# Kernel tuning notes

Measured on AMD Instinct MI355X. Metric: run time of the kernel, lower is better.

The kernel has to match this reference:

```python
import jax, jax.numpy as jnp
import numpy as np

DIM = 512
NUM_HEADS = 4
SCALE = 1.0 / np.sqrt(DIM)  # note: module scales by 1/sqrt(dim), not 1/sqrt(head_dim)


def setup_inputs() -> dict:
    key = jax.random.key(0)
    k1, k2, k3, k4, k5, k6 = jax.random.split(key, 6)
    B, N, M, C = 8, 2048, 2048, DIM
    bound = 1.0 / np.sqrt(C)
    return {
        "F1": jax.random.normal(k1, (B, N, C), dtype=jnp.float32),
        "F2": jax.random.normal(k2, (B, M, C), dtype=jnp.float32),
        "W_qkv": jax.random.uniform(k3, (C, C), jnp.float32, -bound, bound),
        "b_qkv": jax.random.uniform(k4, (C,), jnp.float32, -bound, bound),
        "W_proj": jax.random.uniform(k5, (C, C), jnp.float32, -bound, bound),
        "b_proj": jax.random.uniform(k6, (C,), jnp.float32, -bound, bound),
    }


def reference(F1, F2, W_qkv, b_qkv, W_proj, b_proj):
    B, N, C = F1.shape
    M = F2.shape[1]
    H, D = NUM_HEADS, C // NUM_HEADS
    # shared qkv projection (same weights for q, k and v in the original module)
    q = (F1 @ W_qkv + b_qkv).reshape(B, N, H, D)  # queries from F1
    kv = (F2 @ W_qkv + b_qkv).reshape(B, M, H, D)  # keys == values from F2
    attn = jnp.einsum("bnhd,bmhd->bhnm", q * SCALE, kv)
    attn = jax.nn.softmax(attn, axis=-1)
    x = jnp.einsum("bhnm,bmhd->bnhd", attn, kv).reshape(B, N, C)
    return x @ W_proj + b_proj
```

## Files before the change

kernel.cpp:

```cpp
#include <hip/hip_runtime.h>
#include <math.h>


typedef __attribute__((ext_vector_type(8))) short s16x8;
typedef __attribute__((ext_vector_type(4))) float f32x4;

#define C_DIM 512
#define HDIM  128
#define NROWS 16384
#define SCALE_Q 0.04419417382415922f
#define LOG2E   1.4426950408889634f

__device__ __forceinline__ unsigned short f2bf(float f) {
    union { float f; unsigned u; } v; v.f = f;
    unsigned r = v.u + 0x7fffu + ((v.u >> 16) & 1u);
    return (unsigned short)(r >> 16);
}

__device__ __forceinline__ void async16(const void* g, void* l) {
    __builtin_amdgcn_global_load_lds(
        (const __attribute__((address_space(1))) void*)g,
        (__attribute__((address_space(3))) void*)l, 16, 0, 0);
}

__global__ __launch_bounds__(256)
void conv_bf16_2(const float* __restrict__ s0, const float* __restrict__ s1,
                 unsigned short* __restrict__ d0, unsigned short* __restrict__ d1,
                 int n8) {
    const float* src = blockIdx.y ? s1 : s0;
    unsigned short* dst = blockIdx.y ? d1 : d0;
    int i = blockIdx.x * 256 + threadIdx.x;
    if (i >= n8) return;
    float4 a = ((const float4*)src)[2 * i];
    float4 b = ((const float4*)src)[2 * i + 1];
    union { unsigned short us[8]; uint4 v; } o;
    o.us[0] = f2bf(a.x); o.us[1] = f2bf(a.y); o.us[2] = f2bf(a.z); o.us[3] = f2bf(a.w);
    o.us[4] = f2bf(b.x); o.us[5] = f2bf(b.y); o.us[6] = f2bf(b.z); o.us[7] = f2bf(b.w);
    ((uint4*)dst)[i] = o.v;
}

__global__ __launch_bounds__(256)
void wconv_t2(const float* __restrict__ W0, const float* __restrict__ W1,
              unsigned short* __restrict__ T0, unsigned short* __restrict__ T1) {
    const float* W = blockIdx.z ? W1 : W0;
    unsigned short* Wt = blockIdx.z ? T1 : T0;
    __shared__ float t[64][65];
    const int k0 = blockIdx.y * 64, n0 = blockIdx.x * 64;
    const int c = threadIdx.x & 63, r0 = threadIdx.x >> 6;
#pragma unroll
    for (int r = r0; r < 64; r += 4)
        t[r][c] = W[(size_t)(k0 + r) * C_DIM + n0 + c];
    __syncthreads();
#pragma unroll
    for (int r = r0; r < 64; r += 4)
        Wt[(size_t)(n0 + r) * C_DIM + k0 + c] = f2bf(t[c][r]);
}

__global__ __launch_bounds__(256)
void kv_transpose(const unsigned short* __restrict__ KV,
                  unsigned short* __restrict__ KVT) {
    __shared__ unsigned short t[64][66];
    const int key0 = blockIdx.x * 64;
    const int d0   = blockIdx.y * 64;
    const int bh   = blockIdx.z;
    const int b    = bh >> 2, h = bh & 3;
    const int c = threadIdx.x & 63, r0 = threadIdx.x >> 6;
    const unsigned short* src = KV + ((size_t)(b * 2048 + key0)) * C_DIM + h * HDIM + d0;
#pragma unroll
    for (int r = r0; r < 64; r += 4)
        t[r][c] = src[(size_t)r * C_DIM + c];
    __syncthreads();
    unsigned short* dst = KVT + ((size_t)(bh * HDIM + d0)) * 2048 + key0;
#pragma unroll
    for (int r = r0; r < 64; r += 4)
        dst[(size_t)r * 2048 + c] = t[c][r];
}

template <int OUT_BF16>
__global__ __launch_bounds__(256, 3)
void gemm_bt(const unsigned short* __restrict__ A,
             const unsigned short* __restrict__ Bt,
             const float* __restrict__ bias,
             void* __restrict__ Cv, float oscTop, int topRows) {
    __shared__ __align__(16) unsigned short As[128][64];
    __shared__ __align__(16) unsigned short Bs[128][64];

    const int tid  = threadIdx.x;
    const int wid  = tid >> 6;
    const int lane = tid & 63;
    const int lr   = lane & 15;
    const int quad = lane >> 4;
    const int wm   = wid >> 1;
    const int wn   = wid & 1;
    const int rowBase = blockIdx.y * 128;
    const int colBase = blockIdx.x * 128;
    const int srow = lane >> 3;
    const int soff = srow * C_DIM + (((lane & 7) ^ (srow & 7)) * 8);
    const float osc = (rowBase < topRows) ? oscTop : 1.0f;

    f32x4 acc[4][4];
#pragma unroll
    for (int i = 0; i < 4; i++)
#pragma unroll
        for (int j = 0; j < 4; j++) acc[i][j] = (f32x4)0.0f;

    for (int kt = 0; kt < 8; kt++) {
        const int k0 = kt * 64;
        __syncthreads();
#pragma unroll
        for (int i = 0; i < 4; i++) {
            const int R = wid * 32 + i * 8;
            async16(A  + (size_t)(rowBase + R) * C_DIM + k0 + soff, &As[R][0]);
            async16(Bt + (size_t)(colBase + R) * C_DIM + k0 + soff, &Bs[R][0]);
        }
        __syncthreads();

#pragma unroll
        for (int s = 0; s < 2; s++) {
            s16x8 af[4], bf[4];
#pragma unroll
            for (int i = 0; i < 4; i++)
                af[i] = *(const s16x8*)&As[wm * 64 + i * 16 + lr][((s * 4 + quad) ^ (lr & 7)) * 8];
#pragma unroll
            for (int j = 0; j < 4; j++)
                bf[j] = *(const s16x8*)&Bs[wn * 64 + j * 16 + lr][((s * 4 + quad) ^ (lr & 7)) * 8];
#pragma unroll
            for (int i = 0; i < 4; i++)
#pragma unroll
                for (int j = 0; j < 4; j++)
                    acc[i][j] = __builtin_amdgcn_mfma_f32_16x16x32_bf16(af[i], bf[j], acc[i][j], 0, 0, 0);
        }
    }

    float bcol[4];
#pragma unroll
    for (int j = 0; j < 4; j++)
        bcol[j] = bias[colBase + wn * 64 + j * 16 + lr];
#pragma unroll
    for (int i = 0; i < 4; i++) {
#pragma unroll
        for (int j = 0; j < 4; j++) {
            const int col = colBase + wn * 64 + j * 16 + lr;
#pragma unroll
            for (int r = 0; r < 4; r++) {
                const int row = rowBase + wm * 64 + i * 16 + quad * 4 + r;
                float v = (acc[i][j][r] + bcol[j]) * osc;
                if (OUT_BF16)
                    ((unsigned short*)Cv)[(size_t)row * C_DIM + col] = f2bf(v);
                else
                    ((float*)Cv)[(size_t)row * C_DIM + col] = v;
            }
        }
    }
}

__global__ __launch_bounds__(512, 2)
void cross_attn(const unsigned short* __restrict__ Q,
                const unsigned short* __restrict__ KV,
                const unsigned short* __restrict__ KVT,
                unsigned short* __restrict__ X) {
    __shared__ __align__(16) unsigned short Kt[4][64][128];
    __shared__ __align__(16) unsigned short Vt[4][128][64];

    const int tid  = threadIdx.x;
    const int wid  = tid >> 6;
    const int lane = tid & 63;
    const int lr   = lane & 15;
    const int quad = lane >> 4;

    const int wg   = blockIdx.x;
    const int xcd  = wg & 7;
    const int slot = wg >> 3;
    const int p    = xcd + 8 * (slot & 3);
    const int xblk = slot >> 2;
    const int b    = p >> 2;
    const int h    = p & 3;
    const int hoff = h * HDIM;
    const size_t qrow0  = (size_t)b * 2048 + xblk * 256 + wid * 32;
    const size_t kvrow0 = (size_t)b * 2048;

    s16x8 qf[2][4];
#pragma unroll
    for (int i = 0; i < 2; i++)
#pragma unroll
        for (int kk = 0; kk < 4; kk++)
            qf[i][kk] = *(const s16x8*)(Q + (qrow0 + i * 16 + lr) * C_DIM + hoff + kk * 32 + quad * 8);

    const unsigned short* pK[2];
    const unsigned short* pV[2];
#pragma unroll
    for (int a = 0; a < 2; a++) {
        const int R   = wid * 8 + a * 4 + (lane >> 4);
        const int key = 32 * (R >> 5) + 8 * ((R >> 2) & 3) + 4 * ((R >> 4) & 1) + (R & 3);
        const int pp  = lane & 15;
        const int ck  = (pp & 8) | ((pp ^ (R & 7)) & 7);
        pK[a] = KV + (kvrow0 + key) * C_DIM + hoff + ck * 8;
        const int d  = wid * 16 + a * 8 + (lane >> 3);
        const int cv = (lane & 7) ^ (lane >> 3);
        pV[a] = KVT + ((size_t)((b * 4 + h) * HDIM + d)) * 2048 + cv * 8;
    }

    f32x4 O[2][8];
#pragma unroll
    for (int i = 0; i < 2; i++)
#pragma unroll
        for (int dt = 0; dt < 8; dt++) O[i][dt] = (f32x4)0.0f;
    float lacc[2];
    lacc[0] = 0.0f; lacc[1] = 0.0f;

    auto STAGE = [&](int t, int buf) {
        const size_t key0 = (size_t)t * 64;
#pragma unroll
        for (int a = 0; a < 2; a++) {
            async16(pK[a] + key0 * C_DIM, &Kt[buf][wid * 8 + a * 4][0]);
            async16(pV[a] + key0,         &Vt[buf][wid * 16 + a * 8][0]);
        }
    };

    auto COMPUTE = [&](int cur) {
        f32x4 s[2][4];
#pragma unroll
        for (int i = 0; i < 2; i++)
#pragma unroll
            for (int j = 0; j < 4; j++) s[i][j] = (f32x4)0.0f;
        __builtin_amdgcn_s_setprio(1);
#pragma unroll
        for (int kk = 0; kk < 4; kk++) {
#pragma unroll
            for (int j = 0; j < 4; j++) {
                s16x8 kf = *(const s16x8*)&Kt[cur][j * 16 + lr][((kk * 4 + quad) ^ (lr & 7)) * 8];
                s[0][j] = __builtin_amdgcn_mfma_f32_16x16x32_bf16(kf, qf[0][kk], s[0][j], 0, 0, 0);
                s[1][j] = __builtin_amdgcn_mfma_f32_16x16x32_bf16(kf, qf[1][kk], s[1][j], 0, 0, 0);
            }
        }
        __builtin_amdgcn_s_setprio(0);

        s16x8 pa[2][2];
#pragma unroll
        for (int i = 0; i < 2; i++) {
#pragma unroll
            for (int kk = 0; kk < 2; kk++) {
                float p0 = __builtin_amdgcn_exp2f(s[i][2 * kk][0]);
                float p1 = __builtin_amdgcn_exp2f(s[i][2 * kk][1]);
                float p2 = __builtin_amdgcn_exp2f(s[i][2 * kk][2]);
                float p3 = __builtin_amdgcn_exp2f(s[i][2 * kk][3]);
                float p4 = __builtin_amdgcn_exp2f(s[i][2 * kk + 1][0]);
                float p5 = __builtin_amdgcn_exp2f(s[i][2 * kk + 1][1]);
                float p6 = __builtin_amdgcn_exp2f(s[i][2 * kk + 1][2]);
                float p7 = __builtin_amdgcn_exp2f(s[i][2 * kk + 1][3]);
                lacc[i] += ((p0 + p1) + (p2 + p3)) + ((p4 + p5) + (p6 + p7));
                union { unsigned short us[8]; s16x8 v; } pu;
                pu.us[0] = f2bf(p0); pu.us[1] = f2bf(p1);
                pu.us[2] = f2bf(p2); pu.us[3] = f2bf(p3);
                pu.us[4] = f2bf(p4); pu.us[5] = f2bf(p5);
                pu.us[6] = f2bf(p6); pu.us[7] = f2bf(p7);
                pa[i][kk] = pu.v;
            }
        }

        __builtin_amdgcn_s_setprio(1);
#pragma unroll
        for (int kk = 0; kk < 2; kk++) {
#pragma unroll
            for (int dt = 0; dt < 8; dt++) {
                s16x8 vf = *(const s16x8*)&Vt[cur][dt * 16 + lr][((kk * 4 + quad) ^ (lr & 7)) * 8];
                O[0][dt] = __builtin_amdgcn_mfma_f32_16x16x32_bf16(pa[0][kk], vf, O[0][dt], 0, 0, 0);
                O[1][dt] = __builtin_amdgcn_mfma_f32_16x16x32_bf16(pa[1][kk], vf, O[1][dt], 0, 0, 0);
            }
        }
        __builtin_amdgcn_s_setprio(0);
    };

    STAGE(0, 0);
    STAGE(1, 1);

#pragma unroll 4
    for (int kt = 0; kt < 28; kt++) {
        STAGE(kt + 2, (kt + 2) & 3);
        asm volatile("s_waitcnt vmcnt(8)" ::: "memory");
        __builtin_amdgcn_sched_barrier(0);
        __builtin_amdgcn_s_barrier();
        __builtin_amdgcn_sched_barrier(0);
        COMPUTE(kt & 3);
    }
    STAGE(30, 2);
    asm volatile("s_waitcnt vmcnt(8)" ::: "memory");
    __builtin_amdgcn_sched_barrier(0);
    __builtin_amdgcn_s_barrier();
    __builtin_amdgcn_sched_barrier(0);
    COMPUTE(0);

    STAGE(31, 3);
    asm volatile("s_waitcnt vmcnt(8)" ::: "memory");
    __builtin_amdgcn_sched_barrier(0);
    __builtin_amdgcn_s_barrier();
    __builtin_amdgcn_sched_barrier(0);
    COMPUTE(1);

    asm volatile("s_waitcnt vmcnt(4)" ::: "memory");
    __builtin_amdgcn_sched_barrier(0);
    __builtin_amdgcn_s_barrier();
    __builtin_amdgcn_sched_barrier(0);
    COMPUTE(2);

    asm volatile("s_waitcnt vmcnt(0)" ::: "memory");
    __builtin_amdgcn_sched_barrier(0);
    __builtin_amdgcn_s_barrier();
    __builtin_amdgcn_sched_barrier(0);
    COMPUTE(3);

#pragma unroll
    for (int i = 0; i < 2; i++) {
        float l = lacc[i];
        l += __shfl_xor(l, 16);
        l += __shfl_xor(l, 32);
#pragma unroll
        for (int r = 0; r < 4; r++) {
            const float inv = 1.0f / __shfl(l, quad * 4 + r);
            const size_t row = (qrow0 + i * 16 + quad * 4 + r) * C_DIM + hoff;
#pragma unroll
            for (int dt = 0; dt < 8; dt++)
                X[row + dt * 16 + lr] = f2bf(O[i][dt][r] * inv);
        }
    }
}

extern "C" void kernel_launch(void* const* d_in, const int* in_sizes, int n_in,
                              void* d_out, int out_size, void* d_ws, size_t ws_size,
                              hipStream_t stream) {
    const float* F1     = (const float*)d_in[0];
    const float* F2     = (const float*)d_in[1];
    const float* W_qkv  = (const float*)d_in[2];
    const float* b_qkv  = (const float*)d_in[3];
    const float* W_proj = (const float*)d_in[4];
    const float* b_proj = (const float*)d_in[5];
    float* out = (float*)d_out;

    const size_t NC = (size_t)NROWS * C_DIM;
    unsigned short* F1b = (unsigned short*)d_ws;
    unsigned short* F2b = F1b + NC;
    unsigned short* Qw  = F2b + NC;
    unsigned short* KVw = Qw  + NC;
    unsigned short* Wqt = KVw + NC;
    unsigned short* Wpt = Wqt + C_DIM * C_DIM;
    unsigned short* Xw  = F1b;
    unsigned short* KVT = F2b;

    dim3 blk(256);

    conv_bf16_2<<<dim3(NC / 8 / 256, 2), blk, 0, stream>>>(F1, F2, F1b, F2b, (int)(NC / 8));
    wconv_t2<<<dim3(8, 8, 2), blk, 0, stream>>>(W_qkv, W_proj, Wqt, Wpt);

    gemm_bt<1><<<dim3(4, 256), blk, 0, stream>>>(F1b, Wqt, b_qkv, Qw, SCALE_Q * LOG2E, NROWS);
    kv_transpose<<<dim3(32, 2, 32), blk, 0, stream>>>(KVw, KVT);
    cross_attn<<<dim3(256), dim3(512), 0, stream>>>(Qw, KVw, KVT, Xw);
    gemm_bt<0><<<dim3(4, 128), blk, 0, stream>>>(Xw, Wpt, b_proj, out, 1.0f, 0);
}
```

Baseline: 239.3 us.

## Double-buffer GEMM LDS tiles and remap workgroups across XCDs

The projection GEMM now keeps two LDS buffers for A and B tiles. It prefetches the next k-slice with async global-to-LDS loads while computing the current one, using a partial vmcnt wait and split barriers, and raises wave priority around the MFMA section. Grids are flattened to 1D with an XCD-aware mapping so that neighbouring row tiles sharing weight columns land on the same XCD. LDS use doubles and launch bounds drop from 3 to 2 blocks per CU, which trades occupancy for overlap.

```diff
diff --git a/kernel.cpp b/kernel.cpp
--- a/kernel.cpp
+++ b/kernel.cpp
@@ -77,13 +77,13 @@
 }
 
 template <int OUT_BF16>
-__global__ __launch_bounds__(256, 3)
+__global__ __launch_bounds__(256, 2)
 void gemm_bt(const unsigned short* __restrict__ A,
              const unsigned short* __restrict__ Bt,
              const float* __restrict__ bias,
              void* __restrict__ Cv, float oscTop, int topRows) {
-    __shared__ __align__(16) unsigned short As[128][64];
-    __shared__ __align__(16) unsigned short Bs[128][64];
+    __shared__ __align__(16) unsigned short As[2][128][64];
+    __shared__ __align__(16) unsigned short Bs[2][128][64];
 
     const int tid  = threadIdx.x;
     const int wid  = tid >> 6;
@@ -92,8 +92,15 @@
     const int quad = lane >> 4;
     const int wm   = wid >> 1;
     const int wn   = wid & 1;
-    const int rowBase = blockIdx.y * 128;
-    const int colBase = blockIdx.x * 128;
+
+    const int wg   = blockIdx.x;
+    const int xcd  = wg & 7;
+    const int s_   = wg >> 3;
+    const int xblk = s_ & 3;
+    const int y    = xcd + 8 * (s_ >> 2);
+    const int rowBase = y * 128;
+    const int colBase = xblk * 128;
+
     const int srow = lane >> 3;
     const int soff = srow * C_DIM + (((lane & 7) ^ (srow & 7)) * 8);
     const float osc = (rowBase < topRows) ? oscTop : 1.0f;
@@ -104,32 +111,52 @@
 #pragma unroll
         for (int j = 0; j < 4; j++) acc[i][j] = (f32x4)0.0f;
 
-    for (int kt = 0; kt < 8; kt++) {
+    auto STAGE = [&](int kt, int buf) {
         const int k0 = kt * 64;
-        __syncthreads();
 #pragma unroll
         for (int i = 0; i < 4; i++) {
             const int R = wid * 32 + i * 8;
-            async16(A  + (size_t)(rowBase + R) * C_DIM + k0 + soff, &As[R][0]);
-            async16(Bt + (size_t)(colBase + R) * C_DIM + k0 + soff, &Bs[R][0]);
-        }
-        __syncthreads();
-
+            async16(A  + (size_t)(rowBase + R) * C_DIM + k0 + soff, &As[buf][R][0]);
+            async16(Bt + (size_t)(colBase + R) * C_DIM + k0 + soff, &Bs[buf][R][0]);
+        }
+    };
+
+    auto COMPUTE = [&](int buf) {
+        __builtin_amdgcn_s_setprio(1);
 #pragma unroll
         for (int s = 0; s < 2; s++) {
             s16x8 af[4], bf[4];
 #pragma unroll
             for (int i = 0; i < 4; i++)
-                af[i] = *(const s16x8*)&As[wm * 64 + i * 16 + lr][((s * 4 + quad) ^ (lr & 7)) * 8];
+                af[i] = *(const s16x8*)&As[buf][wm * 64 + i * 16 + lr][((s * 4 + quad) ^ (lr & 7)) * 8];
 #pragma unroll
             for (int j = 0; j < 4; j++)
-                bf[j] = *(const s16x8*)&Bs[wn * 64 + j * 16 + lr][((s * 4 + quad) ^ (lr & 7)) * 8];
+                bf[j] = *(const s16x8*)&Bs[buf][wn * 64 + j * 16 + lr][((s * 4 + quad) ^ (lr & 7)) * 8];
 #pragma unroll
             for (int i = 0; i < 4; i++)
 #pragma unroll
                 for (int j = 0; j < 4; j++)
                     acc[i][j] = __builtin_amdgcn_mfma_f32_16x16x32_bf16(af[i], bf[j], acc[i][j], 0, 0, 0);
         }
+        __builtin_amdgcn_s_setprio(0);
+    };
+
+    STAGE(0, 0);
+#pragma unroll 2
+    for (int kt = 0; kt < 8; kt++) {
+        __builtin_amdgcn_sched_barrier(0);
+        __builtin_amdgcn_s_barrier();
+        __builtin_amdgcn_sched_barrier(0);
+        if (kt < 7) {
+            STAGE(kt + 1, (kt + 1) & 1);
+            asm volatile("s_waitcnt vmcnt(8)" ::: "memory");
+        } else {
+            asm volatile("s_waitcnt vmcnt(0)" ::: "memory");
+        }
+        __builtin_amdgcn_sched_barrier(0);
+        __builtin_amdgcn_s_barrier();
+        __builtin_amdgcn_sched_barrier(0);
+        COMPUTE(kt & 1);
     }
 
     float bcol[4];
@@ -351,8 +378,8 @@
     conv_bf16_2<<<dim3(NC / 8 / 256, 2), blk, 0, stream>>>(F1, F2, F1b, F2b, (int)(NC / 8));
     wconv_t2<<<dim3(8, 8, 2), blk, 0, stream>>>(W_qkv, W_proj, Wqt, Wpt);
 
-    gemm_bt<1><<<dim3(4, 256), blk, 0, stream>>>(F1b, Wqt, b_qkv, Qw, SCALE_Q * LOG2E, NROWS);
+    gemm_bt<1><<<dim3(1024), blk, 0, stream>>>(F1b, Wqt, b_qkv, Qw, SCALE_Q * LOG2E, NROWS);
     kv_transpose<<<dim3(32, 2, 32), blk, 0, stream>>>(KVw, KVT);
     cross_attn<<<dim3(256), dim3(512), 0, stream>>>(Qw, KVw, KVT, Xw);
-    gemm_bt<0><<<dim3(4, 128), blk, 0, stream>>>(Xw, Wpt, b_proj, out, 1.0f, 0);
-}
+    gemm_bt<0><<<dim3(512), blk, 0, stream>>>(Xw, Wpt, b_proj, out, 1.0f, 0);
+}
```

New measurement: 240.9 us. About the same (+0.7%).
